# Kernel tuning notes

Measured on AMD Instinct MI355X. Metric: run time of the kernel, lower is better.

## Reference

```python
import jax, jax.numpy as jnp
import numpy as np

N = 100000   # nodes
E = 1600000  # edges
G = 256      # graphs
NF = 7       # node features
EF = 3       # edge features (in/out)
UD = 2       # global feature dim
H = 128      # hidden dim
NL = 2       # MetaLayers = n_layers - 1
DOUT = 1


def _lin_init(k, fan_in, fan_out):
    return jax.random.normal(k, (fan_in, fan_out), jnp.float32) / np.sqrt(fan_in)


def _mlp2(h, W1, b1, W2, b2):
    return jax.nn.relu(h @ W1 + b1) @ W2 + b2


def setup_inputs() -> dict:
    key = jax.random.key(0)
    ks = jax.random.split(key, 40)
    x = jax.random.normal(ks[0], (N, NF), jnp.float32)
    edge_index = jax.random.randint(ks[1], (2, E), 0, N, jnp.int64)
    edge_attr = jax.random.normal(ks[2], (E, EF), jnp.float32)
    u = jax.random.normal(ks[3], (G, UD), jnp.float32)
    batch = jnp.sort(jax.random.randint(ks[4], (N,), 0, G, jnp.int64))
    # stacked per-layer params (NL identical layers)
    e_in = 2 * NF + EF          # 17
    n_in = NF + 3 * EF + UD     # 18
    eW1 = jnp.stack([_lin_init(ks[5 + i], e_in, H) for i in range(NL)])
    eb1 = jnp.zeros((NL, H), jnp.float32)
    eW2 = jnp.stack([_lin_init(ks[7 + i], H, EF) for i in range(NL)])
    eb2 = jnp.zeros((NL, EF), jnp.float32)
    nW1 = jnp.stack([_lin_init(ks[9 + i], n_in, H) for i in range(NL)])
    nb1 = jnp.zeros((NL, H), jnp.float32)
    nW2 = jnp.stack([_lin_init(ks[11 + i], H, NF) for i in range(NL)])
    nb2 = jnp.zeros((NL, NF), jnp.float32)
    # output head: 3*node_out + global_in -> H -> H -> H -> dim_out
    oW1 = _lin_init(ks[20], 3 * NF + UD, H); ob1 = jnp.zeros((H,), jnp.float32)
    oW2 = _lin_init(ks[21], H, H); ob2 = jnp.zeros((H,), jnp.float32)
    oW3 = _lin_init(ks[22], H, H); ob3 = jnp.zeros((H,), jnp.float32)
    oW4 = _lin_init(ks[23], H, DOUT); ob4 = jnp.zeros((DOUT,), jnp.float32)
    return dict(x=x, edge_attr=edge_attr, u=u,
                eW1=eW1, eb1=eb1, eW2=eW2, eb2=eb2,
                nW1=nW1, nb1=nb1, nW2=nW2, nb2=nb2,
                oW1=oW1, ob1=ob1, oW2=oW2, ob2=ob2,
                oW3=oW3, ob3=ob3, oW4=oW4, ob4=ob4,
                edge_index=edge_index, batch=batch)


def _segment_reduce3(vals, seg, num):
    # add / max (empty -> 0, matching torch_scatter fill) / mean
    s = jax.ops.segment_sum(vals, seg, num_segments=num)
    cnt = jax.ops.segment_sum(jnp.ones((vals.shape[0], 1), vals.dtype), seg, num_segments=num)
    m = jax.ops.segment_max(vals, seg, num_segments=num)
    m = jnp.where(cnt > 0, m, jnp.zeros_like(m))
    mean = s / jnp.maximum(cnt, 1.0)
    return s, m, mean, cnt


def reference(x, edge_attr, u, eW1, eb1, eW2, eb2, nW1, nb1, nW2, nb2,
              oW1, ob1, oW2, ob2, oW3, ob3, oW4, ob4, edge_index, batch):
    row, col = edge_index[0], edge_index[1]
    for l in range(NL):
        # EdgeModel: gather src/dest node feats + edge feats -> MLP
        e_in = jnp.concatenate([x[row], x[col], edge_attr], axis=1)  # [E, 2*NF+EF]
        edge_attr = _mlp2(e_in, eW1[l], eb1[l], eW2[l], eb2[l])      # [E, EF]
        # NodeModel: three scatter reductions over incoming edges (col)
        s, m, mean, _ = _segment_reduce3(edge_attr, col, N)
        n_in = jnp.concatenate([x, s, m, mean, u[batch]], axis=1)    # [N, NF+3*EF+UD]
        x = _mlp2(n_in, nW1[l], nb1[l], nW2[l], nb2[l])              # [N, NF]
    # global pools per graph
    s, m, mean, _ = _segment_reduce3(x, batch, G)
    h = jnp.concatenate([s, mean, m, u], axis=1)                     # [G, 3*NF+UD]
    h = jax.nn.relu(h @ oW1 + ob1)
    h = jax.nn.relu(h @ oW2 + ob2)
    h = jax.nn.relu(h @ oW3 + ob3)
    return h @ oW4 + ob4                                             # [G, DOUT]
```

## Files before the change

### kernel.cpp

```cpp
#include <hip/hip_runtime.h>

#define NN 100000
#define NE 1600000
#define NG 256
#define NB 391
#define NBH 1024
#define CHUNK 1563
#define NBINS 1024
#define NBUCK 782

typedef __attribute__((ext_vector_type(8))) short short8v;
typedef __attribute__((ext_vector_type(4))) float float4v;

__device__ __forceinline__ unsigned short f2bf(float f) {
    unsigned u = __float_as_uint(f);
    return (unsigned short)((u + 0x7FFFu + ((u >> 16) & 1u)) >> 16);
}
__device__ __forceinline__ unsigned fenc(float f) {
    unsigned u = __float_as_uint(f);
    return (u & 0x80000000u) ? ~u : (u | 0x80000000u);
}
__device__ __forceinline__ float fdec(unsigned e) {
    return __uint_as_float((e & 0x80000000u) ? (e & 0x7FFFFFFFu) : ~e);
}

__global__ __launch_bounds__(256) void hist_kernel(
    const int* __restrict__ col, unsigned* __restrict__ ghist) {
    __shared__ unsigned h[NBINS];
    int b = blockIdx.x;
    for (int i = threadIdx.x; i < NBINS; i += 256) h[i] = 0;
    __syncthreads();
    int e0 = b * CHUNK;
    int e1 = e0 + CHUNK; if (e1 > NE) e1 = NE;
    for (int e = e0 + threadIdx.x; e < e1; e += 256)
        atomicAdd(&h[col[e] >> 7], 1u);
    __syncthreads();
    for (int i = threadIdx.x; i < NBINS; i += 256)
        ghist[(size_t)b * NBINS + i] = h[i];
}

__global__ __launch_bounds__(1024) void scanB_kernel(
    const unsigned* __restrict__ ghist, unsigned* __restrict__ goff,
    unsigned* __restrict__ total) {
    __shared__ unsigned a[NBH], bb[NBH];
    int bin = blockIdx.x, t = threadIdx.x;
    unsigned v = ghist[(size_t)t * NBINS + bin];
    a[t] = v;
    __syncthreads();
    unsigned* src = a; unsigned* dst = bb;
    for (int off = 1; off < NBH; off <<= 1) {
        unsigned x = src[t];
        if (t >= off) x += src[t - off];
        dst[t] = x;
        __syncthreads();
        unsigned* tmp = src; src = dst; dst = tmp;
    }
    goff[(size_t)t * NBINS + bin] = src[t] - v;
    if (t == NBH - 1) total[bin] = src[t];
}

__global__ __launch_bounds__(1024) void scanC_kernel(
    const unsigned* __restrict__ total, unsigned* __restrict__ binbase) {
    __shared__ unsigned a[NBINS], bb[NBINS];
    int t = threadIdx.x;
    unsigned v = total[t];
    a[t] = v;
    __syncthreads();
    unsigned* src = a; unsigned* dst = bb;
    for (int off = 1; off < NBINS; off <<= 1) {
        unsigned x = src[t];
        if (t >= off) x += src[t - off];
        dst[t] = x;
        __syncthreads();
        unsigned* tmp = src; src = dst; dst = tmp;
    }
    binbase[t] = src[t] - v;
    if (t == NBINS - 1) binbase[NBINS] = src[t];
}

__global__ __launch_bounds__(256) void scatterD_kernel(
    const int* __restrict__ row, const int* __restrict__ col,
    const float* __restrict__ ea,
    const unsigned* __restrict__ goff, const unsigned* __restrict__ binbase,
    int2* __restrict__ rcT, float* __restrict__ eabT) {
    __shared__ unsigned cur[NBINS];
    int b = blockIdx.x;
    for (int i = threadIdx.x; i < NBINS; i += 256) cur[i] = 0;
    __syncthreads();
    int e0 = b * CHUNK;
    int e1 = e0 + CHUNK; if (e1 > NE) e1 = NE;
    const unsigned* grow = goff + (size_t)b * NBINS;
    for (int e = e0 + threadIdx.x; e < e1; e += 256) {
        int c = col[e];
        int bin = c >> 7;
        unsigned l = atomicAdd(&cur[bin], 1u);
        unsigned slot = binbase[bin] + grow[bin] + l;
        rcT[slot] = make_int2(row[e], c);
        eabT[(size_t)slot * 3 + 0] = ea[(size_t)e * 3 + 0];
        eabT[(size_t)slot * 3 + 1] = ea[(size_t)e * 3 + 1];
        eabT[(size_t)slot * 3 + 2] = ea[(size_t)e * 3 + 2];
    }
}

__global__ __launch_bounds__(256) void bucketsort_kernel(
    const int2* __restrict__ rcT, const float* __restrict__ eabT,
    const unsigned* __restrict__ binbase,
    int2* __restrict__ rc, float* __restrict__ eab, unsigned* __restrict__ start)
{
    __shared__ unsigned lcnt[128], sa[128], sb[128], lcur[128];
    int bin = blockIdx.x, tid = threadIdx.x;
    if (tid < 128) lcnt[tid] = 0;
    __syncthreads();
    unsigned beg = binbase[bin], end = binbase[bin + 1];
    for (unsigned k = beg + tid; k < end; k += 256)
        atomicAdd(&lcnt[rcT[k].y & 127], 1u);
    __syncthreads();
    if (tid < 128) sa[tid] = lcnt[tid];
    __syncthreads();
    unsigned* src = sa; unsigned* dst = sb;
    for (int off = 1; off < 128; off <<= 1) {
        if (tid < 128) {
            unsigned v = src[tid];
            if (tid >= off) v += src[tid - off];
            dst[tid] = v;
        }
        __syncthreads();
        unsigned* t2 = src; src = dst; dst = t2;
    }
    if (tid < 128) {
        unsigned excl = src[tid] - lcnt[tid];
        lcur[tid] = excl;
        int n = (bin << 7) + tid;
        if (n < NN) {
            start[n] = beg + excl;
            if (n == NN - 1) start[NN] = beg + excl + lcnt[tid];
        }
    }
    __syncthreads();
    for (unsigned k = beg + tid; k < end; k += 256) {
        int2 p = rcT[k];
        unsigned l = atomicAdd(&lcur[p.y & 127], 1u);
        unsigned slot = beg + l;
        rc[slot] = p;
        eab[(size_t)slot * 3 + 0] = eabT[(size_t)k * 3 + 0];
        eab[(size_t)slot * 3 + 1] = eabT[(size_t)k * 3 + 1];
        eab[(size_t)slot * 3 + 2] = eabT[(size_t)k * 3 + 2];
    }
}

__global__ __launch_bounds__(256) void gbound_kernel(
    const int* __restrict__ batch, int* __restrict__ gstart) {
    int n = blockIdx.x * 256 + threadIdx.x;
    if (n >= NN) return;
    int b = batch[n];
    int bp = (n == 0) ? -1 : batch[n - 1];
    for (int g = bp + 1; g <= b; ++g) gstart[g] = n;
    if (n == NN - 1) {
        for (int g = b + 1; g <= NG; ++g) gstart[g] = NN;
    }
}

__global__ __launch_bounds__(256) void prep_kernel(
    const float* __restrict__ eW1, const float* __restrict__ eb1, const float* __restrict__ eW2,
    const float* __restrict__ nW1, const float* __restrict__ nb1, const float* __restrict__ nW2,
    short* __restrict__ ewf, float* __restrict__ w2f, float* __restrict__ b1f,
    float* __restrict__ nwt)
{
    int t = blockIdx.x * 256 + threadIdx.x;
    const int EWF = 2 * 4096;
    const int W2F = 2 * 1536;
    const int B1F = 2 * 512;
    const int NWT = 2 * 128 * 28;
    if (t < EWF) {
        int layer = t >> 12, r = t & 4095;
        int tt = r >> 9, r2 = r & 511;
        int l = r2 >> 3, i = r2 & 7;
        int kk = ((l >> 4) << 3) + i;
        int n = tt * 16 + (l & 15);
        float v = (kk < 17) ? eW1[layer * 17 * 128 + kk * 128 + n] : 0.f;
        ewf[t] = (short)f2bf(v);
    } else if (t < EWF + W2F) {
        int q = t - EWF;
        int layer = q / 1536, r = q % 1536;
        int l = r / 24, r2 = r % 24;
        int tt = r2 / 3, c = r2 % 3;
        int k = tt * 16 + (l & 15);
        w2f[q] = eW2[layer * 384 + k * 3 + c];
    } else if (t < EWF + W2F + B1F) {
        int q = t - EWF - W2F;
        int layer = q / 512, r = q % 512;
        int l = r / 8, tt = r % 8;
        b1f[q] = eb1[layer * 128 + tt * 16 + (l & 15)];
    } else if (t < EWF + W2F + B1F + NWT) {
        int q = t - EWF - W2F - B1F;
        int l = q / (128 * 28), rest = q % (128 * 28), j = rest / 28, i = rest % 28;
        float v = 0.f;
        if (i < 18)       v = nW1[l * 18 * 128 + i * 128 + j];
        else if (i == 18) v = nb1[l * 128 + j];
        else if (i < 26)  v = nW2[l * 128 * 7 + j * 7 + (i - 19)];
        nwt[q] = v;
    }
}

__global__ __launch_bounds__(256) void edge_kernel(
    const float* __restrict__ x, float* eab,
    const int2* __restrict__ rc,
    const short* __restrict__ ewf, const float* __restrict__ w2f,
    const float* __restrict__ b1f, const float* __restrict__ b2)
{
    int lane = threadIdx.x & 63;
    int l15 = lane & 15, lg = lane >> 4;
    int wid = (blockIdx.x * 256 + threadIdx.x) >> 6;
    int nwaves = gridDim.x * 4;

    short8v B1[8];
    #pragma unroll
    for (int t = 0; t < 8; ++t)
        B1[t] = *(const short8v*)(ewf + (t * 64 + lane) * 8);
    float w2a[8], w2b[8], w2c[8], b1v[8];
    #pragma unroll
    for (int t = 0; t < 8; ++t) {
        w2a[t] = w2f[lane * 24 + t * 3 + 0];
        w2b[t] = w2f[lane * 24 + t * 3 + 1];
        w2c[t] = w2f[lane * 24 + t * 3 + 2];
        b1v[t] = b1f[lane * 8 + t];
    }
    float bb0 = b2[0], bb1 = b2[1], bb2 = b2[2];

    const int NT = NE / 16;
    for (int tile = wid; tile < NT; tile += nwaves) {
        int s = tile * 16 + l15;
        int2 p = rc[s];
        const float* xr = x + (size_t)p.x * 7;
        const float* xc = x + (size_t)p.y * 7;
        const float* ep = eab + (size_t)s * 3;

        float av0 = 0.f, av1 = 0.f, av2 = 0.f, av3 = 0.f,
              av4 = 0.f, av5 = 0.f, av6 = 0.f, av7 = 0.f;
        if (lg == 0) {
            av0 = xr[0]; av1 = xr[1]; av2 = xr[2]; av3 = xr[3];
            av4 = xr[4]; av5 = xr[5]; av6 = xr[6]; av7 = xc[0];
        } else if (lg == 1) {
            av0 = xc[1]; av1 = xc[2]; av2 = xc[3]; av3 = xc[4];
            av4 = xc[5]; av5 = xc[6]; av6 = ep[0]; av7 = ep[1];
        } else if (lg == 2) {
            av0 = ep[2];
        }

        short8v A;
        A[0] = (short)f2bf(av0); A[1] = (short)f2bf(av1);
        A[2] = (short)f2bf(av2); A[3] = (short)f2bf(av3);
        A[4] = (short)f2bf(av4); A[5] = (short)f2bf(av5);
        A[6] = (short)f2bf(av6); A[7] = (short)f2bf(av7);

        float4v Z = {0.f, 0.f, 0.f, 0.f};
        float4v C[8];
        #pragma unroll
        for (int t = 0; t < 8; ++t)
            C[t] = __builtin_amdgcn_mfma_f32_16x16x32_bf16(A, B1[t], Z, 0, 0, 0);

        float p00 = 0.f, p01 = 0.f, p02 = 0.f;
        float p10 = 0.f, p11 = 0.f, p12 = 0.f;
        float p20 = 0.f, p21 = 0.f, p22 = 0.f;
        float p30 = 0.f, p31 = 0.f, p32 = 0.f;
        #pragma unroll
        for (int t = 0; t < 8; ++t) {
            float h0 = fmaxf(C[t][0] + b1v[t], 0.f);
            float h1 = fmaxf(C[t][1] + b1v[t], 0.f);
            float h2 = fmaxf(C[t][2] + b1v[t], 0.f);
            float h3 = fmaxf(C[t][3] + b1v[t], 0.f);
            p00 += h0 * w2a[t]; p01 += h0 * w2b[t]; p02 += h0 * w2c[t];
            p10 += h1 * w2a[t]; p11 += h1 * w2b[t]; p12 += h1 * w2c[t];
            p20 += h2 * w2a[t]; p21 += h2 * w2b[t]; p22 += h2 * w2c[t];
            p30 += h3 * w2a[t]; p31 += h3 * w2b[t]; p32 += h3 * w2c[t];
        }
        #pragma unroll
        for (int m = 1; m < 16; m <<= 1) {
            p00 += __shfl_xor(p00, m, 16); p01 += __shfl_xor(p01, m, 16); p02 += __shfl_xor(p02, m, 16);
            p10 += __shfl_xor(p10, m, 16); p11 += __shfl_xor(p11, m, 16); p12 += __shfl_xor(p12, m, 16);
            p20 += __shfl_xor(p20, m, 16); p21 += __shfl_xor(p21, m, 16); p22 += __shfl_xor(p22, m, 16);
            p30 += __shfl_xor(p30, m, 16); p31 += __shfl_xor(p31, m, 16); p32 += __shfl_xor(p32, m, 16);
        }
        if (l15 < 4) {
            float o0 = (l15 == 0) ? p00 : (l15 == 1) ? p10 : (l15 == 2) ? p20 : p30;
            float o1 = (l15 == 0) ? p01 : (l15 == 1) ? p11 : (l15 == 2) ? p21 : p31;
            float o2 = (l15 == 0) ? p02 : (l15 == 1) ? p12 : (l15 == 2) ? p22 : p32;
            size_t off = (size_t)(tile * 16 + lg * 4 + l15) * 3;
            eab[off + 0] = o0 + bb0;
            eab[off + 1] = o1 + bb1;
            eab[off + 2] = o2 + bb2;
        }
    }
}

__global__ __launch_bounds__(256) void reduce_kernel(
    const float* __restrict__ eab, const unsigned* __restrict__ start,
    const float* __restrict__ u, const int* __restrict__ batch,
    float* __restrict__ nred)
{
    int gid = blockIdx.x * 256 + threadIdx.x;
    int n = gid >> 4, sub = gid & 15;
    if (n >= NN) return;
    unsigned sbeg = start[n], send = start[n + 1];

    float s0 = 0.f, s1 = 0.f, s2 = 0.f;
    float m0 = -__builtin_inff(), m1 = -__builtin_inff(), m2 = -__builtin_inff();
    for (unsigned k = sbeg + sub; k < send; k += 16) {
        float v0 = eab[(size_t)k * 3 + 0];
        float v1 = eab[(size_t)k * 3 + 1];
        float v2 = eab[(size_t)k * 3 + 2];
        s0 += v0; s1 += v1; s2 += v2;
        m0 = fmaxf(m0, v0); m1 = fmaxf(m1, v1); m2 = fmaxf(m2, v2);
    }
    #pragma unroll
    for (int msk = 1; msk < 16; msk <<= 1) {
        s0 += __shfl_xor(s0, msk, 16);
        s1 += __shfl_xor(s1, msk, 16);
        s2 += __shfl_xor(s2, msk, 16);
        m0 = fmaxf(m0, __shfl_xor(m0, msk, 16));
        m1 = fmaxf(m1, __shfl_xor(m1, msk, 16));
        m2 = fmaxf(m2, __shfl_xor(m2, msk, 16));
    }
    if (sub == 0) {
        float deg = (float)(send - sbeg);
        if (send == sbeg) { m0 = 0.f; m1 = 0.f; m2 = 0.f; }
        float inv = 1.f / fmaxf(deg, 1.f);
        int b = batch[n];
        float* o = nred + (size_t)n * 12;
        o[0] = s0; o[1] = s1; o[2] = s2;
        o[3] = m0; o[4] = m1; o[5] = m2;
        o[6] = s0 * inv; o[7] = s1 * inv; o[8] = s2 * inv;
        o[9] = u[b * 2 + 0]; o[10] = u[b * 2 + 1];
    }
}

#define NMLP_BLOCKS 1024
#define NMLP_WAVES (NMLP_BLOCKS * 4)
__global__ __launch_bounds__(256, 4) void nodemlp_kernel(
    const float* x_in, const float* __restrict__ nred,
    const float* __restrict__ wt, const float* __restrict__ b2,
    float* x_out)
{
    int lane = threadIdx.x & 63;
    int wid = (blockIdx.x * 256 + threadIdx.x) >> 6;

    const float* ra = wt + lane * 28;
    const float* rb = wt + (lane + 64) * 28;
    float a0 = ra[0], a1 = ra[1], a2 = ra[2], a3 = ra[3], a4 = ra[4], a5 = ra[5],
          a6 = ra[6], a7 = ra[7], a8 = ra[8], a9 = ra[9], a10 = ra[10], a11 = ra[11],
          a12 = ra[12], a13 = ra[13], a14 = ra[14], a15 = ra[15], a16 = ra[16], a17 = ra[17],
          ab = ra[18], p0 = ra[19], p1 = ra[20], p2 = ra[21], p3 = ra[22], p4 = ra[23],
          p5 = ra[24], p6 = ra[25];
    float b0 = rb[0], b1 = rb[1], b2_ = rb[2], b3 = rb[3], b4 = rb[4], b5 = rb[5],
          b6 = rb[6], b7 = rb[7], b8 = rb[8], b9 = rb[9], b10 = rb[10], b11 = rb[11],
          b12 = rb[12], b13 = rb[13], b14 = rb[14], b15 = rb[15], b16 = rb[16], b17 = rb[17],
          bb = rb[18], q0 = rb[19], q1 = rb[20], q2 = rb[21], q3 = rb[22], q4 = rb[23],
          q5 = rb[24], q6 = rb[25];

    asm volatile("" : "+v"(a0), "+v"(a1), "+v"(a2), "+v"(a3), "+v"(a4), "+v"(a5),
                      "+v"(a6), "+v"(a7), "+v"(a8), "+v"(a9), "+v"(a10), "+v"(a11),
                      "+v"(a12), "+v"(a13), "+v"(a14), "+v"(a15), "+v"(a16), "+v"(a17),
                      "+v"(ab), "+v"(p0), "+v"(p1), "+v"(p2), "+v"(p3), "+v"(p4),
                      "+v"(p5), "+v"(p6));
    asm volatile("" : "+v"(b0), "+v"(b1), "+v"(b2_), "+v"(b3), "+v"(b4), "+v"(b5),
                      "+v"(b6), "+v"(b7), "+v"(b8), "+v"(b9), "+v"(b10), "+v"(b11),
                      "+v"(b12), "+v"(b13), "+v"(b14), "+v"(b15), "+v"(b16), "+v"(b17),
                      "+v"(bb), "+v"(q0), "+v"(q1), "+v"(q2), "+v"(q3), "+v"(q4),
                      "+v"(q5), "+v"(q6));

    float B0 = b2[0], B1 = b2[1], B2 = b2[2], B3 = b2[3], B4 = b2[4], B5 = b2[5], B6 = b2[6];

    const int nper = (NN + NMLP_WAVES - 1) / NMLP_WAVES;
    int n0 = wid * nper;
    int n1 = n0 + nper; if (n1 > NN) n1 = NN;

    #pragma unroll 2
    for (int n = n0; n < n1; ++n) {
        int nu = __builtin_amdgcn_readfirstlane(n);
        const float* xp = x_in + (size_t)nu * 7;
        const float* rp = nred + (size_t)nu * 12;
        float i0 = xp[0], i1 = xp[1], i2 = xp[2], i3 = xp[3], i4 = xp[4], i5 = xp[5], i6 = xp[6];
        float s0 = rp[0], s1 = rp[1], s2 = rp[2];
        float m0 = rp[3], m1 = rp[4], m2 = rp[5];
        float e0 = rp[6], e1 = rp[7], e2 = rp[8];
        float u0 = rp[9], u1 = rp[10];

        float ha = ab, hb = bb;
        ha += i0 * a0;  hb += i0 * b0;
        ha += i1 * a1;  hb += i1 * b1;
        ha += i2 * a2;  hb += i2 * b2_;
        ha += i3 * a3;  hb += i3 * b3;
        ha += i4 * a4;  hb += i4 * b4;
        ha += i5 * a5;  hb += i5 * b5;
        ha += i6 * a6;  hb += i6 * b6;
        ha += s0 * a7;  hb += s0 * b7;
        ha += s1 * a8;  hb += s1 * b8;
        ha += s2 * a9;  hb += s2 * b9;
        ha += m0 * a10; hb += m0 * b10;
        ha += m1 * a11; hb += m1 * b11;
        ha += m2 * a12; hb += m2 * b12;
        ha += e0 * a13; hb += e0 * b13;
        ha += e1 * a14; hb += e1 * b14;
        ha += e2 * a15; hb += e2 * b15;
        ha += u0 * a16; hb += u0 * b16;
        ha += u1 * a17; hb += u1 * b17;
        ha = fmaxf(ha, 0.f); hb = fmaxf(hb, 0.f);

        float c0 = ha * p0 + hb * q0;
        float c1 = ha * p1 + hb * q1;
        float c2 = ha * p2 + hb * q2;
        float c3 = ha * p3 + hb * q3;
        float c4 = ha * p4 + hb * q4;
        float c5 = ha * p5 + hb * q5;
        float c6 = ha * p6 + hb * q6;
        #pragma unroll
        for (int msk = 1; msk < 64; msk <<= 1) {
            c0 += __shfl_xor(c0, msk);
            c1 += __shfl_xor(c1, msk);
            c2 += __shfl_xor(c2, msk);
            c3 += __shfl_xor(c3, msk);
            c4 += __shfl_xor(c4, msk);
            c5 += __shfl_xor(c5, msk);
            c6 += __shfl_xor(c6, msk);
        }
        float o = c0 + B0;
        if (lane == 1) o = c1 + B1;
        if (lane == 2) o = c2 + B2;
        if (lane == 3) o = c3 + B3;
        if (lane == 4) o = c4 + B4;
        if (lane == 5) o = c5 + B5;
        if (lane == 6) o = c6 + B6;
        if (lane < 7) x_out[(size_t)nu * 7 + lane] = o;
    }
}

__global__ __launch_bounds__(256) void pool_head_kernel(
    const float* __restrict__ x, const int* __restrict__ gstart,
    const float* __restrict__ u,
    const float* __restrict__ oW1, const float* __restrict__ ob1,
    const float* __restrict__ oW2, const float* __restrict__ ob2,
    const float* __restrict__ oW3, const float* __restrict__ ob3,
    const float* __restrict__ oW4, const float* __restrict__ ob4,
    float* __restrict__ out)
{
    int g = blockIdx.x, tid = threadIdx.x;
    int lane = tid & 63, wv = tid >> 6;
    int gs = gstart[g], ge = gstart[g + 1];

    float s0 = 0.f, s1 = 0.f, s2 = 0.f, s3 = 0.f, s4 = 0.f, s5 = 0.f, s6 = 0.f;
    float m0 = -__builtin_inff(), m1 = m0, m2 = m0, m3 = m0, m4 = m0, m5 = m0, m6 = m0;
    for (int n = gs + tid; n < ge; n += 256) {
        const float* xp = x + (size_t)n * 7;
        float v0 = xp[0], v1 = xp[1], v2 = xp[2], v3 = xp[3], v4 = xp[4], v5 = xp[5], v6 = xp[6];
        s0 += v0; s1 += v1; s2 += v2; s3 += v3; s4 += v4; s5 += v5; s6 += v6;
        m0 = fmaxf(m0, v0); m1 = fmaxf(m1, v1); m2 = fmaxf(m2, v2); m3 = fmaxf(m3, v3);
        m4 = fmaxf(m4, v4); m5 = fmaxf(m5, v5); m6 = fmaxf(m6, v6);
    }
    #pragma unroll
    for (int msk = 1; msk < 64; msk <<= 1) {
        s0 += __shfl_xor(s0, msk); s1 += __shfl_xor(s1, msk); s2 += __shfl_xor(s2, msk);
        s3 += __shfl_xor(s3, msk); s4 += __shfl_xor(s4, msk); s5 += __shfl_xor(s5, msk);
        s6 += __shfl_xor(s6, msk);
        m0 = fmaxf(m0, __shfl_xor(m0, msk)); m1 = fmaxf(m1, __shfl_xor(m1, msk));
        m2 = fmaxf(m2, __shfl_xor(m2, msk)); m3 = fmaxf(m3, __shfl_xor(m3, msk));
        m4 = fmaxf(m4, __shfl_xor(m4, msk)); m5 = fmaxf(m5, __shfl_xor(m5, msk));
        m6 = fmaxf(m6, __shfl_xor(m6, msk));
    }
    __shared__ float red[4][14];
    __shared__ float hin[23];
    __shared__ float ha[128];
    __shared__ float hbuf[128];
    if (lane == 0) {
        red[wv][0] = s0; red[wv][1] = s1; red[wv][2] = s2; red[wv][3] = s3;
        red[wv][4] = s4; red[wv][5] = s5; red[wv][6] = s6;
        red[wv][7] = m0; red[wv][8] = m1; red[wv][9] = m2; red[wv][10] = m3;
        red[wv][11] = m4; red[wv][12] = m5; red[wv][13] = m6;
    }
    __syncthreads();
    if (tid < 7) {
        float S = red[0][tid] + red[1][tid] + red[2][tid] + red[3][tid];
        float M = fmaxf(fmaxf(red[0][7 + tid], red[1][7 + tid]),
                        fmaxf(red[2][7 + tid], red[3][7 + tid]));
        float cntf = (float)(ge - gs);
        if (ge == gs) M = 0.f;
        hin[tid] = S;
        hin[7 + tid] = S / fmaxf(cntf, 1.f);
        hin[14 + tid] = M;
    }
    if (tid < 2) hin[21 + tid] = u[g * 2 + tid];
    __syncthreads();

    float h = 0.f;
    if (tid < 128) {
        h = ob1[tid];
        for (int i = 0; i < 23; ++i) h += hin[i] * oW1[i * 128 + tid];
        ha[tid] = fmaxf(h, 0.f);
    }
    __syncthreads();
    if (tid < 128) {
        h = ob2[tid];
        for (int i = 0; i < 128; ++i) h += ha[i] * oW2[i * 128 + tid];
        hbuf[tid] = fmaxf(h, 0.f);
    }
    __syncthreads();
    if (tid < 128) {
        h = ob3[tid];
        for (int i = 0; i < 128; ++i) h += hbuf[i] * oW3[i * 128 + tid];
        ha[tid] = fmaxf(h, 0.f) * oW4[tid];
    }
    __syncthreads();
    if (tid == 0) {
        float acc = ob4[0];
        for (int i = 0; i < 128; ++i) acc += ha[i];
        out[g] = acc;
    }
}

extern "C" void kernel_launch(void* const* d_in, const int* in_sizes, int n_in,
                              void* d_out, int out_size, void* d_ws, size_t ws_size,
                              hipStream_t stream) {
    const float* x         = (const float*)d_in[0];
    const float* edge_attr = (const float*)d_in[1];
    const float* u         = (const float*)d_in[2];
    const float* eW1 = (const float*)d_in[3];
    const float* eb1 = (const float*)d_in[4];
    const float* eW2 = (const float*)d_in[5];
    const float* eb2 = (const float*)d_in[6];
    const float* nW1 = (const float*)d_in[7];
    const float* nb1 = (const float*)d_in[8];
    const float* nW2 = (const float*)d_in[9];
    const float* nb2 = (const float*)d_in[10];
    const float* oW1 = (const float*)d_in[11];
    const float* ob1 = (const float*)d_in[12];
    const float* oW2 = (const float*)d_in[13];
    const float* ob2 = (const float*)d_in[14];
    const float* oW3 = (const float*)d_in[15];
    const float* ob3 = (const float*)d_in[16];
    const float* oW4 = (const float*)d_in[17];
    const float* ob4 = (const float*)d_in[18];
    const int* edge_index = (const int*)d_in[19];
    const int* batch      = (const int*)d_in[20];
    const int* row = edge_index;
    const int* col = edge_index + NE;

    float* ws        = (float*)d_ws;
    float* eab       = ws;
    float* eabT      = eab + (size_t)NE * 3;
    float* ws_x      = eabT + (size_t)NE * 3;
    int2*  rc        = (int2*)(ws_x + (size_t)NN * 7);
    int2*  rcT       = rc + (size_t)NE;
    float* nred      = (float*)(rcT + (size_t)NE);
    unsigned* ghist  = (unsigned*)(nred + (size_t)NN * 12);
    unsigned* goff   = ghist + (size_t)NBH * NBINS;
    unsigned* total  = goff + (size_t)NBH * NBINS;
    unsigned* binbase = total + NBINS;
    unsigned* startv = binbase + NBINS + 4;
    int* gstart      = (int*)(startv + NN + 4);
    float* nwt       = (float*)(gstart + 260);
    float* w2f       = nwt + 2 * 128 * 28;
    float* b1f       = w2f + 2 * 1536;
    uintptr_t ewb    = ((uintptr_t)(b1f + 2 * 512) + 15) & ~(uintptr_t)15;
    short* ewf       = (short*)ewb;

    dim3 b256(256);
    dim3 gn(NB);

    hist_kernel<<<NBH, b256, 0, stream>>>(col, ghist);
    gbound_kernel<<<gn, b256, 0, stream>>>(batch, gstart);
    scanB_kernel<<<NBINS, 1024, 0, stream>>>(ghist, goff, total);
    scanC_kernel<<<1, 1024, 0, stream>>>(total, binbase);
    scatterD_kernel<<<NBH, b256, 0, stream>>>(row, col, edge_attr, goff, binbase, rcT, eabT);
    bucketsort_kernel<<<NBUCK, b256, 0, stream>>>(rcT, eabT, binbase, rc, eab, startv);

    {
        int t = 2 * 4096 + 2 * 1536 + 2 * 512 + 2 * 128 * 28;
        prep_kernel<<<(t + 255) / 256, b256, 0, stream>>>(
            eW1, eb1, eW2, nW1, nb1, nW2, ewf, w2f, b1f, nwt);
    }

    dim3 gemf(2048);
    dim3 gr((NN * 16 + 255) / 256);

    edge_kernel<<<gemf, b256, 0, stream>>>(x, eab, rc, ewf, w2f, b1f, eb2);
    reduce_kernel<<<gr, b256, 0, stream>>>(eab, startv, u, batch, nred);
    nodemlp_kernel<<<NMLP_BLOCKS, b256, 0, stream>>>(x, nred, nwt, nb2, ws_x);

    edge_kernel<<<gemf, b256, 0, stream>>>(ws_x, eab, rc,
        ewf + 4096, w2f + 1536, b1f + 512, eb2 + 3);
    reduce_kernel<<<gr, b256, 0, stream>>>(eab, startv, u, batch, nred);
    nodemlp_kernel<<<NMLP_BLOCKS, b256, 0, stream>>>(ws_x, nred, nwt + 128 * 28, nb2 + 7, ws_x);

    pool_head_kernel<<<NG, b256, 0, stream>>>(ws_x, gstart, u,
        oW1, ob1, oW2, ob2, oW3, ob3, oW4, ob4, (float*)d_out);
}
```

Baseline: 400.0 us.

## Store edge and node features as padded bf16 for vectorized gathers

Edge attributes are now kept as bf16, padded to 4 shorts, through the sort, edge MLP and reduction stages. Node features get a bf16 copy padded to 8 shorts, written by a new conversion kernel and by the node MLP. The edge kernel can then load its MFMA A operand with one 16-byte load per lane instead of scalar fp32 gathers plus conversions, and the edge-weight packing is remapped to match the padded layout. This cuts gather and stream traffic, at the cost of rounding intermediate edge outputs to bf16 before the sum, max and mean reductions, which may loosen accuracy.

```diff
diff --git a/kernel.cpp b/kernel.cpp
--- a/kernel.cpp
+++ b/kernel.cpp
@@ -10,18 +10,15 @@
 #define NBUCK 782
 
 typedef __attribute__((ext_vector_type(8))) short short8v;
+typedef __attribute__((ext_vector_type(4))) short short4v;
 typedef __attribute__((ext_vector_type(4))) float float4v;
 
 __device__ __forceinline__ unsigned short f2bf(float f) {
     unsigned u = __float_as_uint(f);
     return (unsigned short)((u + 0x7FFFu + ((u >> 16) & 1u)) >> 16);
 }
-__device__ __forceinline__ unsigned fenc(float f) {
-    unsigned u = __float_as_uint(f);
-    return (u & 0x80000000u) ? ~u : (u | 0x80000000u);
-}
-__device__ __forceinline__ float fdec(unsigned e) {
-    return __uint_as_float((e & 0x80000000u) ? (e & 0x7FFFFFFFu) : ~e);
+__device__ __forceinline__ float bf2f(unsigned short s) {
+    return __uint_as_float(((unsigned)s) << 16);
 }
 
 __global__ __launch_bounds__(256) void hist_kernel(
@@ -82,7 +79,7 @@
     const int* __restrict__ row, const int* __restrict__ col,
     const float* __restrict__ ea,
     const unsigned* __restrict__ goff, const unsigned* __restrict__ binbase,
-    int2* __restrict__ rcT, float* __restrict__ eabT) {
+    int2* __restrict__ rcT, unsigned short* __restrict__ eabfT) {
     __shared__ unsigned cur[NBINS];
     int b = blockIdx.x;
     for (int i = threadIdx.x; i < NBINS; i += 256) cur[i] = 0;
@@ -96,16 +93,20 @@
         unsigned l = atomicAdd(&cur[bin], 1u);
         unsigned slot = binbase[bin] + grow[bin] + l;
         rcT[slot] = make_int2(row[e], c);
-        eabT[(size_t)slot * 3 + 0] = ea[(size_t)e * 3 + 0];
-        eabT[(size_t)slot * 3 + 1] = ea[(size_t)e * 3 + 1];
-        eabT[(size_t)slot * 3 + 2] = ea[(size_t)e * 3 + 2];
+        short4v ov;
+        ov[0] = (short)f2bf(ea[(size_t)e * 3 + 0]);
+        ov[1] = (short)f2bf(ea[(size_t)e * 3 + 1]);
+        ov[2] = (short)f2bf(ea[(size_t)e * 3 + 2]);
+        ov[3] = 0;
+        *(short4v*)(eabfT + (size_t)slot * 4) = ov;
     }
 }
 
 __global__ __launch_bounds__(256) void bucketsort_kernel(
-    const int2* __restrict__ rcT, const float* __restrict__ eabT,
+    const int2* __restrict__ rcT, const unsigned short* __restrict__ eabfT,
     const unsigned* __restrict__ binbase,
-    int2* __restrict__ rc, float* __restrict__ eab, unsigned* __restrict__ start)
+    int2* __restrict__ rc, unsigned short* __restrict__ eabf,
+    unsigned* __restrict__ start)
 {
     __shared__ unsigned lcnt[128], sa[128], sb[128], lcur[128];
     int bin = blockIdx.x, tid = threadIdx.x;
@@ -142,9 +143,8 @@
         unsigned l = atomicAdd(&lcur[p.y & 127], 1u);
         unsigned slot = beg + l;
         rc[slot] = p;
-        eab[(size_t)slot * 3 + 0] = eabT[(size_t)k * 3 + 0];
-        eab[(size_t)slot * 3 + 1] = eabT[(size_t)k * 3 + 1];
-        eab[(size_t)slot * 3 + 2] = eabT[(size_t)k * 3 + 2];
+        *(short4v*)(eabf + (size_t)slot * 4) =
+            *(const short4v*)(eabfT + (size_t)k * 4);
     }
 }
 
@@ -158,6 +158,17 @@
     if (n == NN - 1) {
         for (int g = b + 1; g <= NG; ++g) gstart[g] = NN;
     }
+}
+
+__global__ __launch_bounds__(256) void x2bf_kernel(
+    const float* __restrict__ x, unsigned short* __restrict__ xbf) {
+    int n = blockIdx.x * 256 + threadIdx.x;
+    if (n >= NN) return;
+    short8v v;
+    #pragma unroll
+    for (int i = 0; i < 7; ++i) v[i] = (short)f2bf(x[(size_t)n * 7 + i]);
+    v[7] = 0;
+    *(short8v*)(xbf + (size_t)n * 8) = v;
 }
 
 __global__ __launch_bounds__(256) void prep_kernel(
@@ -177,7 +188,11 @@
         int l = r2 >> 3, i = r2 & 7;
         int kk = ((l >> 4) << 3) + i;
         int n = tt * 16 + (l & 15);
-        float v = (kk < 17) ? eW1[layer * 17 * 128 + kk * 128 + n] : 0.f;
+        int orig = -1;
+        if (kk < 7)                  orig = kk;
+        else if (kk >= 8 && kk < 15) orig = kk - 1;
+        else if (kk >= 16 && kk < 19) orig = kk - 2;
+        float v = (orig >= 0) ? eW1[layer * 17 * 128 + orig * 128 + n] : 0.f;
         ewf[t] = (short)f2bf(v);
     } else if (t < EWF + W2F) {
         int q = t - EWF;
@@ -203,7 +218,7 @@
 }
 
 __global__ __launch_bounds__(256) void edge_kernel(
-    const float* __restrict__ x, float* eab,
+    const unsigned short* __restrict__ xbf, unsigned short* eabf,
     const int2* __restrict__ rc,
     const short* __restrict__ ewf, const float* __restrict__ w2f,
     const float* __restrict__ b1f, const float* __restrict__ b2)
@@ -231,27 +246,16 @@
     for (int tile = wid; tile < NT; tile += nwaves) {
         int s = tile * 16 + l15;
         int2 p = rc[s];
-        const float* xr = x + (size_t)p.x * 7;
-        const float* xc = x + (size_t)p.y * 7;
-        const float* ep = eab + (size_t)s * 3;
-
-        float av0 = 0.f, av1 = 0.f, av2 = 0.f, av3 = 0.f,
-              av4 = 0.f, av5 = 0.f, av6 = 0.f, av7 = 0.f;
+
+        short8v A = {0, 0, 0, 0, 0, 0, 0, 0};
         if (lg == 0) {
-            av0 = xr[0]; av1 = xr[1]; av2 = xr[2]; av3 = xr[3];
-            av4 = xr[4]; av5 = xr[5]; av6 = xr[6]; av7 = xc[0];
+            A = *(const short8v*)(xbf + (size_t)p.x * 8);
         } else if (lg == 1) {
-            av0 = xc[1]; av1 = xc[2]; av2 = xc[3]; av3 = xc[4];
-            av4 = xc[5]; av5 = xc[6]; av6 = ep[0]; av7 = ep[1];
+            A = *(const short8v*)(xbf + (size_t)p.y * 8);
         } else if (lg == 2) {
-            av0 = ep[2];
-        }
-
-        short8v A;
-        A[0] = (short)f2bf(av0); A[1] = (short)f2bf(av1);
-        A[2] = (short)f2bf(av2); A[3] = (short)f2bf(av3);
-        A[4] = (short)f2bf(av4); A[5] = (short)f2bf(av5);
-        A[6] = (short)f2bf(av6); A[7] = (short)f2bf(av7);
+            short4v e4 = *(const short4v*)(eabf + (size_t)s * 4);
+            A[0] = e4[0]; A[1] = e4[1]; A[2] = e4[2];
+        }
 
         float4v Z = {0.f, 0.f, 0.f, 0.f};
         float4v C[8];
@@ -285,16 +289,19 @@
             float o0 = (l15 == 0) ? p00 : (l15 == 1) ? p10 : (l15 == 2) ? p20 : p30;
             float o1 = (l15 == 0) ? p01 : (l15 == 1) ? p11 : (l15 == 2) ? p21 : p31;
             float o2 = (l15 == 0) ? p02 : (l15 == 1) ? p12 : (l15 == 2) ? p22 : p32;
-            size_t off = (size_t)(tile * 16 + lg * 4 + l15) * 3;
-            eab[off + 0] = o0 + bb0;
-            eab[off + 1] = o1 + bb1;
-            eab[off + 2] = o2 + bb2;
+            short4v ov;
+            ov[0] = (short)f2bf(o0 + bb0);
+            ov[1] = (short)f2bf(o1 + bb1);
+            ov[2] = (short)f2bf(o2 + bb2);
+            ov[3] = 0;
+            size_t eo = (size_t)(tile * 16 + lg * 4 + l15);
+            *(short4v*)(eabf + eo * 4) = ov;
         }
     }
 }
 
 __global__ __launch_bounds__(256) void reduce_kernel(
-    const float* __restrict__ eab, const unsigned* __restrict__ start,
+    const unsigned short* __restrict__ eabf, const unsigned* __restrict__ start,
     const float* __restrict__ u, const int* __restrict__ batch,
     float* __restrict__ nred)
 {
@@ -306,9 +313,10 @@
     float s0 = 0.f, s1 = 0.f, s2 = 0.f;
     float m0 = -__builtin_inff(), m1 = -__builtin_inff(), m2 = -__builtin_inff();
     for (unsigned k = sbeg + sub; k < send; k += 16) {
-        float v0 = eab[(size_t)k * 3 + 0];
-        float v1 = eab[(size_t)k * 3 + 1];
-        float v2 = eab[(size_t)k * 3 + 2];
+        short4v w = *(const short4v*)(eabf + (size_t)k * 4);
+        float v0 = bf2f((unsigned short)w[0]);
+        float v1 = bf2f((unsigned short)w[1]);
+        float v2 = bf2f((unsigned short)w[2]);
         s0 += v0; s1 += v1; s2 += v2;
         m0 = fmaxf(m0, v0); m1 = fmaxf(m1, v1); m2 = fmaxf(m2, v2);
     }
@@ -339,7 +347,7 @@
 __global__ __launch_bounds__(256, 4) void nodemlp_kernel(
     const float* x_in, const float* __restrict__ nred,
     const float* __restrict__ wt, const float* __restrict__ b2,
-    float* x_out)
+    float* x_out, unsigned short* __restrict__ xbf_out)
 {
     int lane = threadIdx.x & 63;
     int wid = (blockIdx.x * 256 + threadIdx.x) >> 6;
@@ -430,7 +438,11 @@
         if (lane == 4) o = c4 + B4;
         if (lane == 5) o = c5 + B5;
         if (lane == 6) o = c6 + B6;
-        if (lane < 7) x_out[(size_t)nu * 7 + lane] = o;
+        if (lane < 7) {
+            x_out[(size_t)nu * 7 + lane] = o;
+            xbf_out[(size_t)nu * 8 + lane] = f2bf(o);
+        }
+        if (lane == 7) xbf_out[(size_t)nu * 8 + 7] = 0;
     }
 }
 
@@ -543,34 +555,37 @@
     const int* row = edge_index;
     const int* col = edge_index + NE;
 
-    float* ws        = (float*)d_ws;
-    float* eab       = ws;
-    float* eabT      = eab + (size_t)NE * 3;
-    float* ws_x      = eabT + (size_t)NE * 3;
-    int2*  rc        = (int2*)(ws_x + (size_t)NN * 7);
-    int2*  rcT       = rc + (size_t)NE;
-    float* nred      = (float*)(rcT + (size_t)NE);
-    unsigned* ghist  = (unsigned*)(nred + (size_t)NN * 12);
-    unsigned* goff   = ghist + (size_t)NBH * NBINS;
-    unsigned* total  = goff + (size_t)NBH * NBINS;
-    unsigned* binbase = total + NBINS;
-    unsigned* startv = binbase + NBINS + 4;
-    int* gstart      = (int*)(startv + NN + 4);
-    float* nwt       = (float*)(gstart + 260);
-    float* w2f       = nwt + 2 * 128 * 28;
-    float* b1f       = w2f + 2 * 1536;
-    uintptr_t ewb    = ((uintptr_t)(b1f + 2 * 512) + 15) & ~(uintptr_t)15;
-    short* ewf       = (short*)ewb;
+    char* base = (char*)d_ws;
+    unsigned short* eabf  = (unsigned short*)base;  base += (size_t)NE * 4 * 2;
+    unsigned short* eabfT = (unsigned short*)base;  base += (size_t)NE * 4 * 2;
+    unsigned short* xbf0  = (unsigned short*)base;  base += (size_t)NN * 8 * 2;
+    unsigned short* xbfA  = (unsigned short*)base;  base += (size_t)NN * 8 * 2;
+    float* xA   = (float*)base;                     base += (size_t)NN * 7 * 4;
+    float* xB   = (float*)base;                     base += (size_t)NN * 7 * 4;
+    int2* rc    = (int2*)base;                      base += (size_t)NE * 8;
+    int2* rcT   = (int2*)base;                      base += (size_t)NE * 8;
+    float* nred = (float*)base;                     base += (size_t)NN * 12 * 4;
+    unsigned* ghist = (unsigned*)base;              base += (size_t)NBH * NBINS * 4;
+    unsigned* goff  = (unsigned*)base;              base += (size_t)NBH * NBINS * 4;
+    unsigned* total = (unsigned*)base;              base += NBINS * 4;
+    unsigned* binbase = (unsigned*)base;            base += (NBINS + 4) * 4;
+    unsigned* startv = (unsigned*)base;             base += (NN + 4) * 4;
+    int* gstart = (int*)base;                       base += 260 * 4;
+    float* nwt = (float*)base;                      base += 2 * 128 * 28 * 4;
+    float* w2f = (float*)base;                      base += 2 * 1536 * 4;
+    float* b1f = (float*)base;                      base += 2 * 512 * 4;
+    short* ewf = (short*)(((uintptr_t)base + 15) & ~(uintptr_t)15);
 
     dim3 b256(256);
     dim3 gn(NB);
 
     hist_kernel<<<NBH, b256, 0, stream>>>(col, ghist);
     gbound_kernel<<<gn, b256, 0, stream>>>(batch, gstart);
+    x2bf_kernel<<<gn, b256, 0, stream>>>(x, xbf0);
     scanB_kernel<<<NBINS, 1024, 0, stream>>>(ghist, goff, total);
     scanC_kernel<<<1, 1024, 0, stream>>>(total, binbase);
-    scatterD_kernel<<<NBH, b256, 0, stream>>>(row, col, edge_attr, goff, binbase, rcT, eabT);
-    bucketsort_kernel<<<NBUCK, b256, 0, stream>>>(rcT, eabT, binbase, rc, eab, startv);
+    scatterD_kernel<<<NBH, b256, 0, stream>>>(row, col, edge_attr, goff, binbase, rcT, eabfT);
+    bucketsort_kernel<<<NBUCK, b256, 0, stream>>>(rcT, eabfT, binbase, rc, eabf, startv);
 
     {
         int t = 2 * 4096 + 2 * 1536 + 2 * 512 + 2 * 128 * 28;
@@ -581,15 +596,16 @@
     dim3 gemf(2048);
     dim3 gr((NN * 16 + 255) / 256);
 
-    edge_kernel<<<gemf, b256, 0, stream>>>(x, eab, rc, ewf, w2f, b1f, eb2);
-    reduce_kernel<<<gr, b256, 0, stream>>>(eab, startv, u, batch, nred);
-    nodemlp_kernel<<<NMLP_BLOCKS, b256, 0, stream>>>(x, nred, nwt, nb2, ws_x);
-
-    edge_kernel<<<gemf, b256, 0, stream>>>(ws_x, eab, rc,
+    edge_kernel<<<gemf, b256, 0, stream>>>(xbf0, eabf, rc, ewf, w2f, b1f, eb2);
+    reduce_kernel<<<gr, b256, 0, stream>>>(eabf, startv, u, batch, nred);
+    nodemlp_kernel<<<NMLP_BLOCKS, b256, 0, stream>>>(x, nred, nwt, nb2, xA, xbfA);
+
+    edge_kernel<<<gemf, b256, 0, stream>>>(xbfA, eabf, rc,
         ewf + 4096, w2f + 1536, b1f + 512, eb2 + 3);
-    reduce_kernel<<<gr, b256, 0, stream>>>(eab, startv, u, batch, nred);
-    nodemlp_kernel<<<NMLP_BLOCKS, b256, 0, stream>>>(ws_x, nred, nwt + 128 * 28, nb2 + 7, ws_x);
-
-    pool_head_kernel<<<NG, b256, 0, stream>>>(ws_x, gstart, u,
+    reduce_kernel<<<gr, b256, 0, stream>>>(eabf, startv, u, batch, nred);
+    nodemlp_kernel<<<NMLP_BLOCKS, b256, 0, stream>>>(xA, nred,
+        nwt + 128 * 28, nb2 + 7, xB, xbfA);
+
+    pool_head_kernel<<<NG, b256, 0, stream>>>(xB, gstart, u,
         oW1, ob1, oW2, ob2, oW3, ob3, oW4, ob4, (float*)d_out);
 }
```

Result: slower. 413.0 us (+3.3%).
